# Kernel tuning notes

Hardware: AMD Instinct MI355X
Metric: run time of the kernel (lower is better)

Reference implementation:

```python
import jax, jax.numpy as jnp
import numpy as np

HEADS = 16
HEAD_DIM = 64
LN_EPS = 1e-5


def setup_inputs() -> dict:
    key = jax.random.key(0)
    k_x, k_q, k_k, k_v = jax.random.split(key, 4)
    B, C, H, W = 32, 640, 32, 32
    inner = HEADS * HEAD_DIM  # 1024
    x = jax.random.normal(k_x, (B, C, H, W), dtype=jnp.float32)
    # nn.Linear(in_dim, inner_dim, bias=False): weight shape [inner, in_dim]
    Wq = jax.random.normal(k_q, (inner, C), dtype=jnp.float32) * 0.02
    Wk = jax.random.normal(k_k, (inner, C), dtype=jnp.float32) * 0.02
    Wv = jax.random.normal(k_v, (inner, C), dtype=jnp.float32) * 0.02
    # out_norm = nn.LayerNorm(head_dim): default init gamma=1, beta=0
    gamma = jnp.ones((HEAD_DIM,), dtype=jnp.float32)
    beta = jnp.zeros((HEAD_DIM,), dtype=jnp.float32)
    return {"x": x, "Wq": Wq, "Wk": Wk, "Wv": Wv, "gamma": gamma, "beta": beta}


def _layernorm(y, gamma, beta):
    mu = jnp.mean(y, axis=-1, keepdims=True)
    var = jnp.mean(jnp.square(y - mu), axis=-1, keepdims=True)
    return (y - mu) * jax.lax.rsqrt(var + LN_EPS) * gamma + beta


def reference(x, Wq, Wk, Wv, gamma, beta):
    B, C, H, W = x.shape
    N = H * W
    scale = HEAD_DIM ** -0.5
    # rearrange 'b c h w -> b (h w) c' (patch_size=1)
    t = x.reshape(B, C, N).transpose(0, 2, 1)  # [B, N, C]
    def proj(Wm):
        p = jnp.einsum('bnc,ec->bne', t, Wm)  # [B, N, inner]
        return p.reshape(B, N, HEADS, HEAD_DIM).transpose(0, 2, 1, 3)  # [B, h, N, d]
    q, k, v = proj(Wq), proj(Wk), proj(Wv)
    qk = jnp.einsum('bhid,bhjd->bhij', q, k)  # [B, h, N, N]
    p_att = jax.nn.softmax(qk * scale, axis=-1)
    out = jnp.einsum('bhij,bhjd->bhid', p_att, v)  # [B, h, N, d]
    out = out.mean(axis=2)  # [B, h, d]
    return _layernorm(out, gamma, beta)
```

## Files before the change

### kernel.cpp

```cpp
#include <hip/hip_runtime.h>
#include <hip/hip_bf16.h>

typedef __bf16 bf16;
typedef __bf16 bf16x8 __attribute__((ext_vector_type(8)));
typedef float f32x4 __attribute__((ext_vector_type(4)));

#define QSCALE 0.18033688011112042f

#define EXP2(x) __builtin_amdgcn_exp2f(x)

__device__ __forceinline__ void load_lds16(const void* gp, void* lp) {
  __builtin_amdgcn_global_load_lds((const __attribute__((address_space(1))) void*)gp,
                                   (__attribute__((address_space(3))) void*)lp, 16, 0, 0);
}

__global__ __launch_bounds__(256) void k_transpose(const float* __restrict__ x,
                                                   bf16* __restrict__ t) {
  __shared__ float tile[64][65];
  const int b = blockIdx.z, c0 = blockIdx.y * 64, n0 = blockIdx.x * 64;
  const int tid = threadIdx.x, lx = tid & 63, ly = tid >> 6;
  const float* xp = x + ((size_t)b * 640 + c0) * 1024 + n0;
#pragma unroll
  for (int i = 0; i < 16; ++i) {
    int c = i * 4 + ly;
    tile[c][lx] = xp[(size_t)c * 1024 + lx];
  }
  __syncthreads();
  bf16* tp = t + ((size_t)b * 1024 + n0) * 640 + c0;
#pragma unroll
  for (int i = 0; i < 16; ++i) {
    int n = i * 4 + ly;
    tp[(size_t)n * 640 + lx] = (bf16)tile[lx][n];
  }
}

__global__ __launch_bounds__(256) void k_castw3(const float* __restrict__ wq,
                                                const float* __restrict__ wk,
                                                const float* __restrict__ wv,
                                                bf16* __restrict__ dst) {
  int i = blockIdx.x * 256 + threadIdx.x;
  if (i < 655360) dst[i] = (bf16)(wq[i] * QSCALE);
  else if (i < 1310720) dst[i] = (bf16)wk[i - 655360];
  else if (i < 1966080) dst[i] = (bf16)wv[i - 1310720];
}

__global__ __launch_bounds__(256) void k_gemm_qkv(const bf16* __restrict__ A,
                                                  const bf16* __restrict__ Bw,
                                                  bf16* __restrict__ qkv) {
  __shared__ __align__(16) bf16 smem[2][2][8192];
  const int tid = threadIdx.x;
  const int lane = tid & 63;
  const int w = tid >> 6;
  const int wm = w & 1, wn = w >> 1;
  const int g = lane >> 4, ln = lane & 15;
  const int m0 = blockIdx.x * 128;
  const int n0 = blockIdx.y * 128;

  f32x4 acc[4][4];
#pragma unroll
  for (int i = 0; i < 4; ++i)
#pragma unroll
    for (int j = 0; j < 4; ++j)
#pragma unroll
      for (int r = 0; r < 4; ++r) acc[i][j][r] = 0.f;

#define GSTAGE(buf, kt)                                                        \
  do {                                                                         \
    _Pragma("unroll") for (int it_ = 0; it_ < 4; ++it_) {                      \
      int c_ = it_ * 256 + w * 64 + lane;                                      \
      int m_ = c_ >> 3;                                                        \
      int kq_ = (c_ & 7) ^ (m_ & 7);                                           \
      load_lds16(A + (size_t)(m0 + m_) * 640 + ((kt) * 64 + kq_ * 8),          \
                 &smem[buf][0][(size_t)(it_ * 256 + w * 64) * 8]);             \
      load_lds16(Bw + (size_t)(n0 + m_) * 640 + ((kt) * 64 + kq_ * 8),        \
                 &smem[buf][1][(size_t)(it_ * 256 + w * 64) * 8]);             \
    }                                                                          \
  } while (0)

  GSTAGE(0, 0);
  for (int kt = 0; kt < 10; ++kt) {
    const int cur = kt & 1;
    __syncthreads();
    if (kt + 1 < 10) GSTAGE(1 - cur, kt + 1);
    const bf16* As = smem[cur][0];
    const bf16* Bs = smem[cur][1];
#pragma unroll
    for (int kk = 0; kk < 2; ++kk) {
      bf16x8 af[4], bfr[4];
#pragma unroll
      for (int mi = 0; mi < 4; ++mi) {
        int m = wm * 64 + mi * 16 + ln;
        int cc = m * 8 + ((kk * 4 + g) ^ (m & 7));
        af[mi] = *(const bf16x8*)(As + cc * 8);
      }
#pragma unroll
      for (int ni = 0; ni < 4; ++ni) {
        int n = wn * 64 + ni * 16 + ln;
        int cc = n * 8 + ((kk * 4 + g) ^ (n & 7));
        bfr[ni] = *(const bf16x8*)(Bs + cc * 8);
      }
#pragma unroll
      for (int mi = 0; mi < 4; ++mi)
#pragma unroll
        for (int ni = 0; ni < 4; ++ni)
          acc[mi][ni] = __builtin_amdgcn_mfma_f32_16x16x32_bf16(af[mi], bfr[ni], acc[mi][ni], 0, 0, 0);
    }
  }
#undef GSTAGE

  __syncthreads();
  bf16* ct = &smem[0][0][0];
#pragma unroll
  for (int mi = 0; mi < 4; ++mi)
#pragma unroll
    for (int ni = 0; ni < 4; ++ni)
#pragma unroll
      for (int r = 0; r < 4; ++r) {
        int row = wm * 64 + mi * 16 + g * 4 + r;
        int col = wn * 64 + ni * 16 + ln;
        ct[row * 136 + col] = (bf16)acc[mi][ni][r];
      }
  __syncthreads();
  const int which = n0 >> 10;
  const int hbase = (n0 >> 6) & 15;
#pragma unroll
  for (int p = 0; p < 8; ++p) {
    int row = p * 16 + (tid >> 4);
    int chunk = tid & 15;
    bf16x8 vv = *(const bf16x8*)(ct + row * 136 + chunk * 8);
    int gr = m0 + row;
    int bb = gr >> 10, n = gr & 1023;
    int h = hbase + (chunk >> 3);
    int d0 = (chunk & 7) * 8;
    *(bf16x8*)(qkv + (size_t)which * 33554432 +
               (((size_t)bb * 16 + h) * 1024 + n) * 64 + d0) = vv;
  }
}

__global__ __launch_bounds__(256) void k_attn(const bf16* __restrict__ q,
                                              const bf16* __restrict__ kmat,
                                              float* __restrict__ wsum) {
  __shared__ __align__(16) bf16 Ks[2][4096];
  const int idx = blockIdx.x;
  const int xcd = idx & 7;
  const int y = idx >> 3;
  const int it = y & 3;
  const int bh = xcd + ((y >> 2) << 3);
  const int tid = threadIdx.x;
  const int lane = tid & 63;
  const int w = tid >> 6;
  const int g = lane >> 4, ln = lane & 15;
  const bf16* qb = q + (size_t)bh * 65536;
  const bf16* kb = kmat + (size_t)bh * 65536;
  const int i0 = it * 256 + w * 64;

  const f32x4 zf = {0.f, 0.f, 0.f, 0.f};

#define STAGEK(buf, jt)                                                       \
  do {                                                                        \
    _Pragma("unroll") for (int call_ = 0; call_ < 2; ++call_) {               \
      int p_ = w * 128 + call_ * 64 + lane;                                   \
      int j_ = p_ >> 3;                                                       \
      int kq_ = (p_ & 7) ^ (j_ & 7);                                          \
      load_lds16(kb + (size_t)((jt) * 64 + j_) * 64 + kq_ * 8,                \
                 &Ks[buf][(size_t)(w * 128 + call_ * 64) * 8]);               \
    }                                                                         \
  } while (0)

#define KFRAG(buf, ni, kc)                                                    \
  (*(const bf16x8*)(&Ks[buf][(size_t)(((ni) * 16 + ln) * 8 +                  \
                                      (((kc) * 4 + g) ^ (ln & 7))) * 8]))

  bf16x8 qf[4][2];
#pragma unroll
  for (int mi = 0; mi < 4; ++mi)
#pragma unroll
    for (int kc = 0; kc < 2; ++kc)
      qf[mi][kc] = *(const bf16x8*)(qb + (size_t)(i0 + mi * 16 + ln) * 64 + kc * 32 + g * 8);

  float rs[4][4];
#pragma unroll
  for (int mi = 0; mi < 4; ++mi)
#pragma unroll
    for (int r = 0; r < 4; ++r) rs[mi][r] = 0.f;

  STAGEK(0, 0);
  for (int jt = 0; jt < 16; ++jt) {
    const int cur = jt & 1;
    __syncthreads();
    if (jt + 1 < 16) STAGEK(1 - cur, jt + 1);
    bf16x8 kf[4][2];
#pragma unroll
    for (int ni = 0; ni < 4; ++ni)
#pragma unroll
      for (int kc = 0; kc < 2; ++kc) kf[ni][kc] = KFRAG(cur, ni, kc);
#pragma unroll
    for (int mi = 0; mi < 4; ++mi)
#pragma unroll
      for (int ni = 0; ni < 4; ++ni) {
        f32x4 s = __builtin_amdgcn_mfma_f32_16x16x32_bf16(qf[mi][0], kf[ni][0], zf, 0, 0, 0);
        s = __builtin_amdgcn_mfma_f32_16x16x32_bf16(qf[mi][1], kf[ni][1], s, 0, 0, 0);
#pragma unroll
        for (int r = 0; r < 4; ++r) rs[mi][r] += EXP2(s[r]);
      }
  }
  float rinv[4][4];
#pragma unroll
  for (int mi = 0; mi < 4; ++mi)
#pragma unroll
    for (int r = 0; r < 4; ++r) {
      float v = rs[mi][r];
      v += __shfl_xor(v, 1);
      v += __shfl_xor(v, 2);
      v += __shfl_xor(v, 4);
      v += __shfl_xor(v, 8);
      rinv[mi][r] = 1.0f / v;
    }

  STAGEK(0, 0);
  for (int jt = 0; jt < 16; ++jt) {
    const int cur = jt & 1;
    __syncthreads();
    if (jt + 1 < 16) STAGEK(1 - cur, jt + 1);
    bf16x8 kf[4][2];
#pragma unroll
    for (int ni = 0; ni < 4; ++ni)
#pragma unroll
      for (int kc = 0; kc < 2; ++kc) kf[ni][kc] = KFRAG(cur, ni, kc);
    float cs[4] = {0.f, 0.f, 0.f, 0.f};
#pragma unroll
    for (int mi = 0; mi < 4; ++mi)
#pragma unroll
      for (int ni = 0; ni < 4; ++ni) {
        f32x4 s = __builtin_amdgcn_mfma_f32_16x16x32_bf16(qf[mi][0], kf[ni][0], zf, 0, 0, 0);
        s = __builtin_amdgcn_mfma_f32_16x16x32_bf16(qf[mi][1], kf[ni][1], s, 0, 0, 0);
#pragma unroll
        for (int r = 0; r < 4; ++r) cs[ni] += EXP2(s[r]) * rinv[mi][r];
      }
#pragma unroll
    for (int ni = 0; ni < 4; ++ni) {
      float v = cs[ni];
      v += __shfl_xor(v, 16);
      v += __shfl_xor(v, 32);
      if (g == 0) atomicAdd(wsum + (size_t)bh * 1024 + jt * 64 + ni * 16 + ln, v);
    }
  }
#undef STAGEK
#undef KFRAG
}

__global__ __launch_bounds__(256) void k_final(const float* __restrict__ wsum,
                                               const bf16* __restrict__ v,
                                               const float* __restrict__ gamma,
                                               const float* __restrict__ beta,
                                               float* __restrict__ out) {
  const int bh = blockIdx.x;
  const int tid = threadIdx.x;
  const int d = tid & 63, part = tid >> 6;
  const bf16* vb = v + (size_t)bh * 65536;
  const float* wb = wsum + (size_t)bh * 1024;
  float acc = 0.f;
  for (int j = part * 256; j < part * 256 + 256; ++j)
    acc += wb[j] * (float)vb[(size_t)j * 64 + d];
  __shared__ float red[4][64];
  red[part][d] = acc;
  __syncthreads();
  if (tid < 64) {
    float y = (red[0][d] + red[1][d] + red[2][d] + red[3][d]) * (1.0f / 1024.0f);
    float s1 = y;
#pragma unroll
    for (int off = 1; off < 64; off <<= 1) s1 += __shfl_xor(s1, off);
    float mu = s1 * (1.0f / 64.0f);
    float dy = y - mu;
    float s2 = dy * dy;
#pragma unroll
    for (int off = 1; off < 64; off <<= 1) s2 += __shfl_xor(s2, off);
    float rstd = rsqrtf(s2 * (1.0f / 64.0f) + 1e-5f);
    out[(size_t)bh * 64 + d] = dy * rstd * gamma[d] + beta[d];
  }
}

extern "C" void kernel_launch(void* const* d_in, const int* in_sizes, int n_in,
                              void* d_out, int out_size, void* d_ws, size_t ws_size,
                              hipStream_t stream) {
  const float* x     = (const float*)d_in[0];
  const float* Wq    = (const float*)d_in[1];
  const float* Wk    = (const float*)d_in[2];
  const float* Wv    = (const float*)d_in[3];
  const float* gamma = (const float*)d_in[4];
  const float* beta  = (const float*)d_in[5];
  float* out = (float*)d_out;

  char* ws = (char*)d_ws;
  bf16*  tbf  = (bf16*)ws;
  bf16*  wbf  = (bf16*)(ws + 41943040);
  bf16*  qkv  = (bf16*)(ws + 45875200);
  float* wsum = (float*)(ws + 247201792);

  hipMemsetAsync(wsum, 0, (size_t)512 * 1024 * sizeof(float), stream);
  k_transpose<<<dim3(16, 10, 32), 256, 0, stream>>>(x, tbf);
  k_castw3<<<7680, 256, 0, stream>>>(Wq, Wk, Wv, wbf);
  k_gemm_qkv<<<dim3(256, 24), 256, 0, stream>>>(tbf, wbf, qkv);
  k_attn<<<2048, 256, 0, stream>>>(qkv, qkv + 33554432, wsum);
  k_final<<<512, 256, 0, stream>>>(wsum, qkv + 67108864, gamma, beta, out);
}
```

Measured before the change: 513.1 us.

## Replace two-pass attention with single-pass fp8-cached probabilities and partial column sums

The attention kernel no longer recomputes QK^T in a second pass. Each block handles a 32-row stripe over all 1024 keys, caches exp2 scores as fp8 in LDS, then computes normalized column sums after a block-wide row-sum reduction. Per-stripe partials are written as bf16 to a workspace buffer instead of using atomics and a memset, and k_final reduces the 32 partials. This halves the MFMA/exp work and removes atomics, at the cost of fp8/bf16 precision loss and more, smaller blocks that load K directly from global memory without LDS staging.

```diff
diff --git a/kernel.cpp b/kernel.cpp
--- a/kernel.cpp
+++ b/kernel.cpp
@@ -4,9 +4,9 @@
 typedef __bf16 bf16;
 typedef __bf16 bf16x8 __attribute__((ext_vector_type(8)));
 typedef float f32x4 __attribute__((ext_vector_type(4)));
+typedef float f32x2 __attribute__((ext_vector_type(2)));
 
 #define QSCALE 0.18033688011112042f
-
 #define EXP2(x) __builtin_amdgcn_exp2f(x)
 
 __device__ __forceinline__ void load_lds16(const void* gp, void* lp) {
@@ -137,132 +137,113 @@
   }
 }
 
-__global__ __launch_bounds__(256) void k_attn(const bf16* __restrict__ q,
-                                              const bf16* __restrict__ kmat,
-                                              float* __restrict__ wsum) {
-  __shared__ __align__(16) bf16 Ks[2][4096];
+__global__ __launch_bounds__(256) void k_attn2(const bf16* __restrict__ q,
+                                               const bf16* __restrict__ kmat,
+                                               bf16* __restrict__ wpart) {
+  __shared__ __align__(16) unsigned char Ps[32768];
+  __shared__ __align__(16) float lpart[2][32];
+  __shared__ float rinvS[32];
   const int idx = blockIdx.x;
   const int xcd = idx & 7;
   const int y = idx >> 3;
-  const int it = y & 3;
-  const int bh = xcd + ((y >> 2) << 3);
+  const int stripe = y & 31;
+  const int bh = xcd + ((y >> 5) << 3);
   const int tid = threadIdx.x;
   const int lane = tid & 63;
   const int w = tid >> 6;
-  const int g = lane >> 4, ln = lane & 15;
+  const int q4 = lane >> 4, ln = lane & 15;
+  const int rg = w & 1, ch = w >> 1;
   const bf16* qb = q + (size_t)bh * 65536;
   const bf16* kb = kmat + (size_t)bh * 65536;
-  const int i0 = it * 256 + w * 64;
-
+  const int i0 = stripe * 32;
   const f32x4 zf = {0.f, 0.f, 0.f, 0.f};
 
-#define STAGEK(buf, jt)                                                       \
-  do {                                                                        \
-    _Pragma("unroll") for (int call_ = 0; call_ < 2; ++call_) {               \
-      int p_ = w * 128 + call_ * 64 + lane;                                   \
-      int j_ = p_ >> 3;                                                       \
-      int kq_ = (p_ & 7) ^ (j_ & 7);                                          \
-      load_lds16(kb + (size_t)((jt) * 64 + j_) * 64 + kq_ * 8,                \
-                 &Ks[buf][(size_t)(w * 128 + call_ * 64) * 8]);               \
-    }                                                                         \
-  } while (0)
-
-#define KFRAG(buf, ni, kc)                                                    \
-  (*(const bf16x8*)(&Ks[buf][(size_t)(((ni) * 16 + ln) * 8 +                  \
-                                      (((kc) * 4 + g) ^ (ln & 7))) * 8]))
-
-  bf16x8 qf[4][2];
-#pragma unroll
-  for (int mi = 0; mi < 4; ++mi)
-#pragma unroll
-    for (int kc = 0; kc < 2; ++kc)
-      qf[mi][kc] = *(const bf16x8*)(qb + (size_t)(i0 + mi * 16 + ln) * 64 + kc * 32 + g * 8);
-
-  float rs[4][4];
-#pragma unroll
-  for (int mi = 0; mi < 4; ++mi)
-#pragma unroll
-    for (int r = 0; r < 4; ++r) rs[mi][r] = 0.f;
-
-  STAGEK(0, 0);
-  for (int jt = 0; jt < 16; ++jt) {
-    const int cur = jt & 1;
-    __syncthreads();
-    if (jt + 1 < 16) STAGEK(1 - cur, jt + 1);
+  const bf16* qp = qb + (size_t)(i0 + rg * 16 + ln) * 64 + q4 * 8;
+  bf16x8 qf0 = *(const bf16x8*)(qp);
+  bf16x8 qf1 = *(const bf16x8*)(qp + 32);
+
+  float rs0 = 0.f, rs1 = 0.f, rs2 = 0.f, rs3 = 0.f;
+
+  for (int jt = 0; jt < 8; ++jt) {
+    const int jbase = ch * 512 + jt * 64;
     bf16x8 kf[4][2];
 #pragma unroll
-    for (int ni = 0; ni < 4; ++ni)
-#pragma unroll
-      for (int kc = 0; kc < 2; ++kc) kf[ni][kc] = KFRAG(cur, ni, kc);
-#pragma unroll
-    for (int mi = 0; mi < 4; ++mi)
-#pragma unroll
-      for (int ni = 0; ni < 4; ++ni) {
-        f32x4 s = __builtin_amdgcn_mfma_f32_16x16x32_bf16(qf[mi][0], kf[ni][0], zf, 0, 0, 0);
-        s = __builtin_amdgcn_mfma_f32_16x16x32_bf16(qf[mi][1], kf[ni][1], s, 0, 0, 0);
-#pragma unroll
-        for (int r = 0; r < 4; ++r) rs[mi][r] += EXP2(s[r]);
-      }
-  }
-  float rinv[4][4];
-#pragma unroll
-  for (int mi = 0; mi < 4; ++mi)
-#pragma unroll
-    for (int r = 0; r < 4; ++r) {
-      float v = rs[mi][r];
-      v += __shfl_xor(v, 1);
-      v += __shfl_xor(v, 2);
-      v += __shfl_xor(v, 4);
-      v += __shfl_xor(v, 8);
-      rinv[mi][r] = 1.0f / v;
-    }
-
-  STAGEK(0, 0);
-  for (int jt = 0; jt < 16; ++jt) {
-    const int cur = jt & 1;
-    __syncthreads();
-    if (jt + 1 < 16) STAGEK(1 - cur, jt + 1);
-    bf16x8 kf[4][2];
-#pragma unroll
-    for (int ni = 0; ni < 4; ++ni)
-#pragma unroll
-      for (int kc = 0; kc < 2; ++kc) kf[ni][kc] = KFRAG(cur, ni, kc);
-    float cs[4] = {0.f, 0.f, 0.f, 0.f};
-#pragma unroll
-    for (int mi = 0; mi < 4; ++mi)
-#pragma unroll
-      for (int ni = 0; ni < 4; ++ni) {
-        f32x4 s = __builtin_amdgcn_mfma_f32_16x16x32_bf16(qf[mi][0], kf[ni][0], zf, 0, 0, 0);
-        s = __builtin_amdgcn_mfma_f32_16x16x32_bf16(qf[mi][1], kf[ni][1], s, 0, 0, 0);
-#pragma unroll
-        for (int r = 0; r < 4; ++r) cs[ni] += EXP2(s[r]) * rinv[mi][r];
-      }
-#pragma unroll
-    for (int ni = 0; ni < 4; ++ni) {
-      float v = cs[ni];
-      v += __shfl_xor(v, 16);
-      v += __shfl_xor(v, 32);
-      if (g == 0) atomicAdd(wsum + (size_t)bh * 1024 + jt * 64 + ni * 16 + ln, v);
-    }
-  }
-#undef STAGEK
-#undef KFRAG
-}
-
-__global__ __launch_bounds__(256) void k_final(const float* __restrict__ wsum,
+    for (int ctl = 0; ctl < 4; ++ctl) {
+      const bf16* kp = kb + (size_t)(jbase + ctl * 16 + ln) * 64 + q4 * 8;
+      kf[ctl][0] = *(const bf16x8*)(kp);
+      kf[ctl][1] = *(const bf16x8*)(kp + 32);
+    }
+#pragma unroll
+    for (int ctl = 0; ctl < 4; ++ctl) {
+      f32x4 s = __builtin_amdgcn_mfma_f32_16x16x32_bf16(qf0, kf[ctl][0], zf, 0, 0, 0);
+      s = __builtin_amdgcn_mfma_f32_16x16x32_bf16(qf1, kf[ctl][1], s, 0, 0, 0);
+      float p0 = EXP2(s[0]), p1 = EXP2(s[1]), p2 = EXP2(s[2]), p3 = EXP2(s[3]);
+      rs0 += p0; rs1 += p1; rs2 += p2; rs3 += p3;
+      int pk = __builtin_amdgcn_cvt_pk_fp8_f32(p0, p1, 0, false);
+      pk = __builtin_amdgcn_cvt_pk_fp8_f32(p2, p3, pk, true);
+      int j = jbase + ctl * 16 + ln;
+      int cc = (rg * 2 + (q4 >> 1)) ^ ((j >> 2) & 3);
+      *(int*)(Ps + j * 32 + cc * 8 + (q4 & 1) * 4) = pk;
+    }
+  }
+  rs0 += __shfl_xor(rs0, 1); rs0 += __shfl_xor(rs0, 2); rs0 += __shfl_xor(rs0, 4); rs0 += __shfl_xor(rs0, 8);
+  rs1 += __shfl_xor(rs1, 1); rs1 += __shfl_xor(rs1, 2); rs1 += __shfl_xor(rs1, 4); rs1 += __shfl_xor(rs1, 8);
+  rs2 += __shfl_xor(rs2, 1); rs2 += __shfl_xor(rs2, 2); rs2 += __shfl_xor(rs2, 4); rs2 += __shfl_xor(rs2, 8);
+  rs3 += __shfl_xor(rs3, 1); rs3 += __shfl_xor(rs3, 2); rs3 += __shfl_xor(rs3, 4); rs3 += __shfl_xor(rs3, 8);
+  if (ln == 0) {
+    f32x4 rr = {rs0, rs1, rs2, rs3};
+    *(f32x4*)&lpart[ch][rg * 16 + q4 * 4] = rr;
+  }
+  __syncthreads();
+  if (tid < 32) rinvS[tid] = 1.0f / (lpart[0][tid] + lpart[1][tid]);
+  __syncthreads();
+
+  bf16* wp = wpart + (size_t)(bh * 32 + stripe) * 1024;
+#pragma unroll
+  for (int k = 0; k < 4; ++k) {
+    int j = w * 256 + k * 64 + lane;
+    int sw = (j >> 2) & 3;
+    float acc = 0.f;
+#pragma unroll
+    for (int c = 0; c < 4; ++c) {
+      const unsigned int* pp = (const unsigned int*)(Ps + j * 32 + ((c ^ sw) << 3));
+      unsigned int lo = pp[0], hi = pp[1];
+      f32x2 a0 = __builtin_amdgcn_cvt_pk_f32_fp8(lo, false);
+      f32x2 a1 = __builtin_amdgcn_cvt_pk_f32_fp8(lo, true);
+      f32x2 a2 = __builtin_amdgcn_cvt_pk_f32_fp8(hi, false);
+      f32x2 a3 = __builtin_amdgcn_cvt_pk_f32_fp8(hi, true);
+      acc += a0.x * rinvS[c * 8 + 0] + a0.y * rinvS[c * 8 + 1]
+           + a1.x * rinvS[c * 8 + 2] + a1.y * rinvS[c * 8 + 3]
+           + a2.x * rinvS[c * 8 + 4] + a2.y * rinvS[c * 8 + 5]
+           + a3.x * rinvS[c * 8 + 6] + a3.y * rinvS[c * 8 + 7];
+    }
+    wp[j] = (bf16)acc;
+  }
+}
+
+__global__ __launch_bounds__(256) void k_final(const bf16* __restrict__ wpart,
                                                const bf16* __restrict__ v,
                                                const float* __restrict__ gamma,
                                                const float* __restrict__ beta,
                                                float* __restrict__ out) {
+  __shared__ float wl[1024];
+  __shared__ float red[4][64];
   const int bh = blockIdx.x;
   const int tid = threadIdx.x;
+  const bf16* wpb = wpart + (size_t)bh * 32768;
+#pragma unroll
+  for (int k = 0; k < 4; ++k) {
+    int j = k * 256 + tid;
+    float a = 0.f;
+    for (int s = 0; s < 32; ++s) a += (float)wpb[s * 1024 + j];
+    wl[j] = a;
+  }
+  __syncthreads();
   const int d = tid & 63, part = tid >> 6;
   const bf16* vb = v + (size_t)bh * 65536;
-  const float* wb = wsum + (size_t)bh * 1024;
   float acc = 0.f;
   for (int j = part * 256; j < part * 256 + 256; ++j)
-    acc += wb[j] * (float)vb[(size_t)j * 64 + d];
-  __shared__ float red[4][64];
+    acc += wl[j] * (float)vb[(size_t)j * 64 + d];
   red[part][d] = acc;
   __syncthreads();
   if (tid < 64) {
@@ -292,15 +273,14 @@
   float* out = (float*)d_out;
 
   char* ws = (char*)d_ws;
-  bf16*  tbf  = (bf16*)ws;
-  bf16*  wbf  = (bf16*)(ws + 41943040);
-  bf16*  qkv  = (bf16*)(ws + 45875200);
-  float* wsum = (float*)(ws + 247201792);
-
-  hipMemsetAsync(wsum, 0, (size_t)512 * 1024 * sizeof(float), stream);
+  bf16*  tbf   = (bf16*)ws;
+  bf16*  wbf   = (bf16*)(ws + 41943040);
+  bf16*  qkv   = (bf16*)(ws + 45875200);
+  bf16*  wpart = (bf16*)ws;
+
   k_transpose<<<dim3(16, 10, 32), 256, 0, stream>>>(x, tbf);
   k_castw3<<<7680, 256, 0, stream>>>(Wq, Wk, Wv, wbf);
   k_gemm_qkv<<<dim3(256, 24), 256, 0, stream>>>(tbf, wbf, qkv);
-  k_attn<<<2048, 256, 0, stream>>>(qkv, qkv + 33554432, wsum);
-  k_final<<<512, 256, 0, stream>>>(wsum, qkv + 67108864, gamma, beta, out);
-}
+  k_attn2<<<16384, 256, 0, stream>>>(qkv, qkv + 33554432, wpart);
+  k_final<<<512, 256, 0, stream>>>(wpart, qkv + 67108864, gamma, beta, out);
+}
```

After: 796.8 us. 1.55x slower.
